# Performance work log

Hardware: AMD Instinct MI355X
Metric: run time of the kernel (lower is better)

The kernel has to match this reference:

```python
import jax, jax.numpy as jnp
import numpy as np

B, S, E, H = 4, 1024, 1024, 16
HD = E // H  # 64


def setup_inputs() -> dict:
    key = jax.random.key(0)
    ks = jax.random.split(key, 9)
    scale = 1.0 / np.sqrt(E)
    x = jax.random.normal(ks[0], (B, S, E), dtype=jnp.float32)
    attention_mask = jnp.ones((B, S, S), dtype=jnp.int32)
    # per-head projection weights, batched over heads: [H, E, HD]
    Wq = jax.random.normal(ks[1], (H, E, HD), dtype=jnp.float32) * scale
    Wk = jax.random.normal(ks[2], (H, E, HD), dtype=jnp.float32) * scale
    Wv = jax.random.normal(ks[3], (H, E, HD), dtype=jnp.float32) * scale
    bq = jax.random.normal(ks[4], (H, HD), dtype=jnp.float32) * scale
    bk = jax.random.normal(ks[5], (H, HD), dtype=jnp.float32) * scale
    bv = jax.random.normal(ks[6], (H, HD), dtype=jnp.float32) * scale
    # output projection, torch Linear convention: [out_features, in_features]
    Wo = jax.random.normal(ks[7], (E, E), dtype=jnp.float32) * scale
    bo = jax.random.normal(ks[8], (E,), dtype=jnp.float32) * scale
    return {"x": x, "attention_mask": attention_mask, "Wq": Wq, "bq": bq,
            "Wk": Wk, "bk": bk, "Wv": Wv, "bv": bv, "Wo": Wo, "bo": bo}


def reference(x, attention_mask, Wq, bq, Wk, bk, Wv, bv, Wo, bo):
    # batched-over-heads QKV projections: (B,S,E) x (H,E,HD) -> (B,H,S,HD)
    q = jnp.einsum('bse,hed->bhsd', x, Wq) + bq[None, :, None, :]
    k = jnp.einsum('bse,hed->bhsd', x, Wk) + bk[None, :, None, :]
    v = jnp.einsum('bse,hed->bhsd', x, Wv) + bv[None, :, None, :]
    scores = jnp.einsum('bhsd,bhtd->bhst', q, k) / jnp.sqrt(jnp.float32(HD))
    mask = attention_mask[:, None, :, :]  # (B,1,S,S) broadcast over heads
    scores = jnp.where(mask == 0, -jnp.inf, scores)
    weights = jax.nn.softmax(scores, axis=-1)
    out = jnp.einsum('bhst,bhtd->bhsd', weights, v)
    # concat heads on last dim: (B,S,H*HD) == (B,S,E)
    out = out.transpose(0, 2, 1, 3).reshape(B, S, E)
    return out @ Wo.T + bo
```

## Files before the change

kernel.cpp:

```cpp
#include <hip/hip_runtime.h>
#include <hip/hip_bf16.h>

#define NB 4
#define SEQ 1024
#define EMB 1024
#define NH 16
#define HD 64

typedef unsigned short u16;
typedef __attribute__((ext_vector_type(8))) __bf16 bf16x8;
typedef __attribute__((ext_vector_type(8))) short short8;
typedef __attribute__((ext_vector_type(4))) float floatx4;

__device__ inline u16 f2b_rn(float f) {
    union { float f; unsigned int i; } x; x.f = f;
    unsigned int r = (x.i + 0x7FFFu + ((x.i >> 16) & 1u)) >> 16;
    return (u16)r;
}
__device__ inline bf16x8 s2b(short8 v) {
    union { short8 s; bf16x8 b; } x; x.s = v; return x.b;
}

__device__ inline void gload_lds16(const void* g, void* l) {
    __builtin_amdgcn_global_load_lds(
        (const __attribute__((address_space(1))) void*)g,
        (__attribute__((address_space(3))) void*)l, 16, 0, 0);
}

__device__ inline bf16x8 ldsfrag(const u16* base, int r, int c) {
    return s2b(*(const short8*)&base[r * 64 + (c ^ ((r & 7) * 8))]);
}

__device__ inline void cvt8(const float* __restrict__ s, u16* __restrict__ d) {
    float4 a = *(const float4*)(s);
    float4 b = *(const float4*)(s + 4);
    union { u16 u[8]; int4 v; } o;
    o.u[0] = f2b_rn(a.x); o.u[1] = f2b_rn(a.y); o.u[2] = f2b_rn(a.z); o.u[3] = f2b_rn(a.w);
    o.u[4] = f2b_rn(b.x); o.u[5] = f2b_rn(b.y); o.u[6] = f2b_rn(b.z); o.u[7] = f2b_rn(b.w);
    *(int4*)(d) = o.v;
}

#define BARX do { __builtin_amdgcn_sched_barrier(0); __builtin_amdgcn_s_barrier(); __builtin_amdgcn_sched_barrier(0); } while(0)
#define VMCNT6 asm volatile("s_waitcnt vmcnt(6)" ::: "memory")
#define VMCNT5 asm volatile("s_waitcnt vmcnt(5)" ::: "memory")
#define VMCNT4 asm volatile("s_waitcnt vmcnt(4)" ::: "memory")
#define VMCNT0 asm volatile("s_waitcnt vmcnt(0)" ::: "memory")

__global__ __launch_bounds__(256) void prep(
    const float* __restrict__ x, const float* __restrict__ Wq,
    const float* __restrict__ Wk, const float* __restrict__ Wv,
    const int* __restrict__ mask,
    u16* __restrict__ xb, u16* __restrict__ Wt,
    unsigned long long* __restrict__ bits)
{
    __shared__ u16 T[64 * 80];
    int bx = blockIdx.x;
    int tid = threadIdx.x;

    if (bx < 512) {
        #pragma unroll
        for (int c = 0; c < 4; ++c) {
            int i = (bx * 4 + c) * 2048 + tid * 8;
            cvt8(x + i, xb + i);
        }
    } else if (bx < 1280) {
        int bx2 = bx - 512;
        int e0 = (bx2 & 15) * 64;
        int ph = bx2 >> 4;
        int p = ph >> 4, h = ph & 15;
        const float* W = (p == 0 ? Wq : (p == 1 ? Wk : Wv)) + h * (EMB * HD);
        #pragma unroll
        for (int c = 0; c < 2; ++c) {
            int flat = c * 2048 + tid * 8;
            int r = flat >> 6;
            int d = flat & 63;
            cvt8(W + (size_t)(e0 + r) * HD + d, &T[r * 80 + d]);
        }
        __syncthreads();
        int d = tid >> 2;
        int ec = tid & 3;
        union { u16 u[16]; int4 v[2]; } tmp;
        #pragma unroll
        for (int i = 0; i < 16; ++i) tmp.u[i] = T[(ec * 16 + i) * 80 + d];
        u16* dst = Wt + ((size_t)(p * NH + h) * HD + d) * EMB + e0 + ec * 16;
        *(int4*)(dst) = tmp.v[0];
        *(int4*)(dst + 8) = tmp.v[1];
    } else {
        int w = tid >> 6, ln = tid & 63;
        int gw = (bx - 1280) * 16 + w * 4 + (ln >> 4);
        int4 v = ((const int4*)mask)[(size_t)gw * 16 + (ln & 15)];
        unsigned nib = (v.x != 0 ? 1u : 0u) | (v.y != 0 ? 2u : 0u)
                     | (v.z != 0 ? 4u : 0u) | (v.w != 0 ? 8u : 0u);
        unsigned long long part = (unsigned long long)nib << ((ln & 15) * 4);
        part |= __shfl_xor(part, 1);
        part |= __shfl_xor(part, 2);
        part |= __shfl_xor(part, 4);
        part |= __shfl_xor(part, 8);
        if ((ln & 15) == 0) bits[gw] = part;
    }
}

__device__ __forceinline__ void rd_b3(const u16* B, int wn, int ln, int quad, bf16x8 (&bfr)[3][2]) {
    #pragma unroll
    for (int nc = 0; nc < 3; ++nc) {
        bfr[nc][0] = ldsfrag(B, wn * 48 + nc * 16 + ln, quad * 8);
        bfr[nc][1] = ldsfrag(B, wn * 48 + nc * 16 + ln, 32 + quad * 8);
    }
}
__device__ __forceinline__ void rd_a(const u16* A, int wm, int mf0, int ln, int quad, bf16x8 (&a)[2][2]) {
    #pragma unroll
    for (int jj = 0; jj < 2; ++jj) {
        a[jj][0] = ldsfrag(A, wm * 128 + (mf0 + jj) * 16 + ln, quad * 8);
        a[jj][1] = ldsfrag(A, wm * 128 + (mf0 + jj) * 16 + ln, 32 + quad * 8);
    }
}
__device__ __forceinline__ void mm12(floatx4 (&acc)[8][3], const bf16x8 (&a)[2][2],
                                     const bf16x8 (&bfr)[3][2], int mf0) {
    #pragma unroll
    for (int jj = 0; jj < 2; ++jj)
        #pragma unroll
        for (int nc = 0; nc < 3; ++nc) {
            acc[mf0 + jj][nc] = __builtin_amdgcn_mfma_f32_16x16x32_bf16(a[jj][0], bfr[nc][0], acc[mf0 + jj][nc], 0, 0, 0);
            acc[mf0 + jj][nc] = __builtin_amdgcn_mfma_f32_16x16x32_bf16(a[jj][1], bfr[nc][1], acc[mf0 + jj][nc], 0, 0, 0);
        }
}

#define STG(srcb, buf, c, kt) gload_lds16((srcb) + (size_t)(c) * 65536 + (kt) * 64 + soff, (buf) + (c) * 4096 + ldst)

__global__ __launch_bounds__(512, 2) void qkv_gemm(
    const u16* __restrict__ x,
    const u16* __restrict__ Wt2,
    const float* __restrict__ bq, const float* __restrict__ bk, const float* __restrict__ bv,
    u16* __restrict__ Q, u16* __restrict__ K, u16* __restrict__ Vt)
{
    __shared__ u16 L[57344];
    u16* A0s = L;
    u16* A1s = L + 16384;
    u16* B0s = L + 32768;
    u16* B1s = L + 45056;

    int gid = blockIdx.x;
    int xcd = gid & 7;
    int j   = gid >> 3;
    int mt_ = (xcd >> 1) * 4 + (j & 3);
    int nt_ = (xcd & 1) * 8 + (j >> 2);
    int m0 = mt_ * 256;
    int n0 = nt_ * 192;

    int tid = threadIdx.x;
    int w = tid >> 6, lane = tid & 63, quad = lane >> 4, ln = lane & 15;
    int wm = w >> 2, wn = w & 3;

    const u16* Asrc = x   + (size_t)m0 * EMB;
    const u16* Bsrc = Wt2 + (size_t)n0 * EMB;

    int sr = tid >> 3;
    int sc = ((tid & 7) ^ (sr & 7)) * 8;
    size_t soff = (size_t)sr * EMB + sc;
    int ldst = w * 512;

    STG(Asrc, A0s, 0, 0); STG(Asrc, A0s, 1, 0); STG(Asrc, A0s, 2, 0); STG(Asrc, A0s, 3, 0);
    STG(Bsrc, B0s, 0, 0); STG(Bsrc, B0s, 1, 0); STG(Bsrc, B0s, 2, 0);
    STG(Bsrc, B1s, 0, 1); STG(Bsrc, B1s, 1, 1); STG(Bsrc, B1s, 2, 1);
    STG(Asrc, A1s, 0, 1); STG(Asrc, A1s, 2, 1);
    VMCNT5;
    BARX;

    floatx4 acc[8][3] = {};
    bf16x8 bfr[3][2];
    bf16x8 a[2][2];

    for (int i = 0; i < 8; ++i) {
        const int T = 2 * i;
        const bool st = (i < 7);
        rd_b3(B0s, wn, ln, quad, bfr);
        rd_a(A0s, wm, 0, ln, quad, a);
        STG(Asrc, A1s, 1, T + 1); STG(Asrc, A1s, 3, T + 1);
        BARX;
        __builtin_amdgcn_s_setprio(1); mm12(acc, a, bfr, 0); __builtin_amdgcn_s_setprio(0);
        BARX;
        rd_a(A0s, wm, 2, ln, quad, a);
        if (st) { STG(Bsrc, B0s, 0, T + 2); STG(Bsrc, B0s, 1, T + 2); }
        BARX;
        __builtin_amdgcn_s_setprio(1); mm12(acc, a, bfr, 2); __builtin_amdgcn_s_setprio(0);
        BARX;
        rd_a(A0s, wm, 4, ln, quad, a);
        if (st) { STG(Bsrc, B0s, 2, T + 2); STG(Asrc, A0s, 0, T + 2); }
        BARX;
        __builtin_amdgcn_s_setprio(1); mm12(acc, a, bfr, 4); __builtin_amdgcn_s_setprio(0);
        BARX;
        rd_a(A0s, wm, 6, ln, quad, a);
        if (st) { STG(Asrc, A0s, 2, T + 2); }
        BARX;
        __builtin_amdgcn_s_setprio(1); mm12(acc, a, bfr, 6); __builtin_amdgcn_s_setprio(0);
        if (st) { VMCNT5; } else { VMCNT0; }
        BARX;
        rd_b3(B1s, wn, ln, quad, bfr);
        rd_a(A1s, wm, 0, ln, quad, a);
        if (st) { STG(Asrc, A0s, 1, T + 2); STG(Asrc, A0s, 3, T + 2); }
        BARX;
        __builtin_amdgcn_s_setprio(1); mm12(acc, a, bfr, 0); __builtin_amdgcn_s_setprio(0);
        BARX;
        rd_a(A1s, wm, 2, ln, quad, a);
        if (st) { STG(Bsrc, B1s, 0, T + 3); STG(Bsrc, B1s, 1, T + 3); }
        BARX;
        __builtin_amdgcn_s_setprio(1); mm12(acc, a, bfr, 2); __builtin_amdgcn_s_setprio(0);
        BARX;
        rd_a(A1s, wm, 4, ln, quad, a);
        if (st) { STG(Bsrc, B1s, 2, T + 3); STG(Asrc, A1s, 0, T + 3); }
        BARX;
        __builtin_amdgcn_s_setprio(1); mm12(acc, a, bfr, 4); __builtin_amdgcn_s_setprio(0);
        BARX;
        rd_a(A1s, wm, 6, ln, quad, a);
        if (st) { STG(Asrc, A1s, 2, T + 3); }
        BARX;
        __builtin_amdgcn_s_setprio(1); mm12(acc, a, bfr, 6); __builtin_amdgcn_s_setprio(0);
        if (st) { VMCNT5; }
        BARX;
    }

    int nb_w = n0 + wn * 48;
    #pragma unroll
    for (int nc = 0; nc < 3; ++nc) {
        int nbc = nb_w + nc * 16;
        int p = nbc >> 10;
        int h = (nbc >> 6) & 15;
        const float* bias = (p == 0 ? bq : (p == 1 ? bk : bv));
        int d = (nbc & 63) + ln;
        float bv_ = bias[(nbc & 1023) + ln];
        if (p < 2) {
            u16* Out = (p == 0) ? Q : K;
            float qs = (p == 0) ? 0.125f * 1.44269504f : 1.0f;
            #pragma unroll
            for (int mf = 0; mf < 8; ++mf) {
                #pragma unroll
                for (int reg = 0; reg < 4; ++reg) {
                    int m = m0 + wm * 128 + mf * 16 + quad * 4 + reg;
                    int b_ = m >> 10, s = m & 1023;
                    Out[((size_t)(b_ * NH + h) * SEQ + s) * HD + d] = f2b_rn((acc[mf][nc][reg] + bv_) * qs);
                }
            }
        } else {
            #pragma unroll
            for (int mf = 0; mf < 8; ++mf) {
                int m = m0 + wm * 128 + mf * 16 + quad * 4;
                int b_ = m >> 10, s = m & 1023;
                union { u16 u[4]; uint2 v; } pk;
                #pragma unroll
                for (int reg = 0; reg < 4; ++reg)
                    pk.u[reg] = f2b_rn(acc[mf][nc][reg] + bv_);
                *(uint2*)&Vt[((size_t)(b_ * NH + h) * HD + d) * SEQ + s] = pk.v;
            }
        }
    }
}

__device__ __forceinline__ void astage512(const u16* __restrict__ Kb, const u16* __restrict__ Vb,
                                          u16* Kd, u16* Vd, int t0, int tid) {
    int r = tid >> 3;
    int c = ((tid & 7) ^ (r & 7)) * 8;
    int base = (tid >> 6) * 512;
    gload_lds16(Kb + (size_t)(t0 + r) * HD + c, Kd + base);
    gload_lds16(Vb + (size_t)r * SEQ + t0 + c, Vd + base);
}

__device__ __forceinline__ void attn_tile(
    const u16* Ksc, const u16* Vsc, u16* Ps,
    const bf16x8 (&qf)[2][2], floatx4 (&o)[2][5],
    unsigned long long bm0, unsigned long long bm1,
    int w, int ln, int quad)
{
    floatx4 sc[2][4] = {};
    #pragma unroll
    for (int kk = 0; kk < 2; ++kk) {
        bf16x8 kf[4];
        #pragma unroll
        for (int tb = 0; tb < 4; ++tb)
            kf[tb] = ldsfrag(Ksc, tb * 16 + ln, kk * 32 + quad * 8);
        __builtin_amdgcn_s_setprio(1);
        #pragma unroll
        for (int s = 0; s < 2; ++s)
            #pragma unroll
            for (int tb = 0; tb < 4; ++tb)
                sc[s][tb] = __builtin_amdgcn_mfma_f32_16x16x32_bf16(kf[tb], qf[s][kk], sc[s][tb], 0, 0, 0);
        __builtin_amdgcn_s_setprio(0);
    }

    #pragma unroll
    for (int s = 0; s < 2; ++s) {
        unsigned long long bm = s ? bm1 : bm0;
        if (__any(bm != ~0ull)) {
            #pragma unroll
            for (int tb = 0; tb < 4; ++tb)
                #pragma unroll
                for (int reg = 0; reg < 4; ++reg)
                    if (!((bm >> (tb * 16 + quad * 4 + reg)) & 1)) sc[s][tb][reg] = -1e30f;
        }
    }

    #pragma unroll
    for (int s = 0; s < 2; ++s) {
        int mrow = w * 32 + s * 16 + ln;
        int swz = (mrow & 7) * 8;
        #pragma unroll
        for (int tb = 0; tb < 4; ++tb) {
            union { float f; unsigned int i; } e0_, e1_, e2_, e3_;
            e0_.f = __builtin_amdgcn_exp2f(sc[s][tb][0]);
            e1_.f = __builtin_amdgcn_exp2f(sc[s][tb][1]);
            e2_.f = __builtin_amdgcn_exp2f(sc[s][tb][2]);
            e3_.f = __builtin_amdgcn_exp2f(sc[s][tb][3]);
            uint2 pk;
            pk.x = ((e0_.i + 0x8000u) >> 16) | ((e1_.i + 0x8000u) & 0xFFFF0000u);
            pk.y = ((e2_.i + 0x8000u) >> 16) | ((e3_.i + 0x8000u) & 0xFFFF0000u);
            *(uint2*)&Ps[mrow * 64 + ((tb * 16 + quad * 4) ^ swz)] = pk;
        }
    }

    #pragma unroll
    for (int kk = 0; kk < 2; ++kk) {
        bf16x8 vf[5];
        #pragma unroll
        for (int dt = 0; dt < 5; ++dt)
            vf[dt] = ldsfrag(Vsc, dt * 16 + ln, kk * 32 + quad * 8);
        #pragma unroll
        for (int s = 0; s < 2; ++s) {
            bf16x8 pf = ldsfrag(Ps, w * 32 + s * 16 + ln, kk * 32 + quad * 8);
            __builtin_amdgcn_s_setprio(1);
            #pragma unroll
            for (int dt = 0; dt < 5; ++dt)
                o[s][dt] = __builtin_amdgcn_mfma_f32_16x16x32_bf16(pf, vf[dt], o[s][dt], 0, 0, 0);
            __builtin_amdgcn_s_setprio(0);
        }
    }
}

__global__ __launch_bounds__(512) void attn(
    const u16* __restrict__ Q, const u16* __restrict__ K, const u16* __restrict__ Vt,
    const unsigned long long* __restrict__ bits,
    const float* __restrict__ Wo, u16* __restrict__ Wob,
    u16* __restrict__ Aout)
{
    __shared__ u16 L[16512 + 256 * 64];
    u16* Ks0 = L;
    u16* Ks1 = L + 4096;
    u16* Vs0 = L + 8192;
    u16* Vs1 = L + 12352;
    u16* Ps  = L + 16512;

    int bid = blockIdx.x;
    int tid = threadIdx.x;

    if (bid >= 256) {
        int i = (bid - 256) * 4096 + tid * 8;
        cvt8(Wo + i, Wob + i);
        return;
    }

    int bh = bid & 63;
    int q0 = (bid >> 6) * 256;
    int b = bh >> 4, h = bh & 15;
    const u16* Qb = Q  + (size_t)bh * SEQ * HD;
    const u16* Kb = K  + (size_t)bh * SEQ * HD;
    const u16* Vb = Vt + (size_t)bh * HD * SEQ;

    int w = tid >> 6, lane = tid & 63, quad = lane >> 4, ln = lane & 15;

    if (tid < 32) {
        u16* dst = (tid < 16 ? L + 12288 : L + 16448) + (tid & 15) * 4;
        *(uint2*)dst = make_uint2(0x3F803F80u, 0x3F803F80u);
    }

    bf16x8 qf[2][2];
    #pragma unroll
    for (int s = 0; s < 2; ++s) {
        const u16* qp = Qb + (size_t)(q0 + w * 32 + s * 16 + ln) * HD + quad * 8;
        union { int4 i; bf16x8 b; } c0, c1;
        c0.i = *(const int4*)(qp);
        c1.i = *(const int4*)(qp + 32);
        qf[s][0] = c0.b; qf[s][1] = c1.b;
    }

    __syncthreads();

    astage512(Kb, Vb, Ks0, Vs0, 0,  tid);
    astage512(Kb, Vb, Ks1, Vs1, 64, tid);
    size_t bb0 = ((size_t)b * SEQ + q0 + w * 32 + ln) * 16;
    size_t bb1 = bb0 + 256;
    unsigned long long bmn0 = bits[bb0];
    unsigned long long bmn1 = bits[bb1];

    floatx4 o[2][5] = {};

    for (int i = 0; i < 8; ++i) {
        VMCNT4;
        BARX;
        {
            unsigned long long bc0 = bmn0, bc1 = bmn1;
            bmn0 = bits[bb0 + (2 * i + 1)];
            bmn1 = bits[bb1 + (2 * i + 1)];
            attn_tile(Ks0, Vs0, Ps, qf, o, bc0, bc1, w, ln, quad);
        }
        BARX;
        if (i < 7) astage512(Kb, Vb, Ks0, Vs0, i * 128 + 128, tid);
        if (i < 7) { VMCNT4; } else { VMCNT0; }
        BARX;
        {
            unsigned long long bc0 = bmn0, bc1 = bmn1;
            if (i < 7) { bmn0 = bits[bb0 + (2 * i + 2)]; bmn1 = bits[bb1 + (2 * i + 2)]; }
            attn_tile(Ks1, Vs1, Ps, qf, o, bc0, bc1, w, ln, quad);
        }
        BARX;
        if (i < 7) astage512(Kb, Vb, Ks1, Vs1, i * 128 + 192, tid);
    }

    #pragma unroll
    for (int s = 0; s < 2; ++s) {
        #pragma unroll
        for (int reg = 0; reg < 4; ++reg) {
            float l = __shfl(o[s][4][reg], lane & 48, 64);
            float inv = 1.0f / l;
            int m = q0 + w * 32 + s * 16 + quad * 4 + reg;
            #pragma unroll
            for (int dt = 0; dt < 4; ++dt)
                Aout[((size_t)b * SEQ + m) * EMB + h * HD + dt * 16 + ln] = f2b_rn(o[s][dt][reg] * inv);
        }
    }
}

#define OSTG_A(buf, kt) gload_lds16(Asrc + (size_t)(kt) * 64 + soff, (buf) + ldst)
#define OSTG_B(buf, c, kt) gload_lds16(Bsrc + (size_t)(c) * 65536 + (size_t)(kt) * 64 + soff, (buf) + (c) * 4096 + ldst)

__device__ __forceinline__ void op_tile(const u16* As, const u16* Bs,
                                        floatx4 (&acc)[4][2], int w, int ln, int quad)
{
    #pragma unroll
    for (int kk = 0; kk < 2; ++kk) {
        bf16x8 av[4], bv2[2];
        #pragma unroll
        for (int mf = 0; mf < 4; ++mf)
            av[mf] = ldsfrag(As, mf * 16 + ln, kk * 32 + quad * 8);
        #pragma unroll
        for (int nc = 0; nc < 2; ++nc)
            bv2[nc] = ldsfrag(Bs, w * 32 + nc * 16 + ln, kk * 32 + quad * 8);
        __builtin_amdgcn_s_setprio(1);
        #pragma unroll
        for (int mf = 0; mf < 4; ++mf)
            #pragma unroll
            for (int nc = 0; nc < 2; ++nc)
                acc[mf][nc] = __builtin_amdgcn_mfma_f32_16x16x32_bf16(av[mf], bv2[nc], acc[mf][nc], 0, 0, 0);
        __builtin_amdgcn_s_setprio(0);
    }
}

__global__ __launch_bounds__(512, 2) void out_proj(
    const u16* __restrict__ A,
    const u16* __restrict__ Wo,
    const float* __restrict__ bo,
    float* __restrict__ Out)
{
    __shared__ u16 L[40960];
    u16* A0s = L;
    u16* A1s = L + 4096;
    u16* B0s = L + 8192;
    u16* B1s = L + 24576;

    int gid = blockIdx.x;
    int xcd = gid & 7;
    int j   = gid >> 3;
    int m0 = (xcd * 8 + (j & 7)) * 64;
    int n0 = (j >> 3) * 256;

    int tid = threadIdx.x;
    int w = tid >> 6, lane = tid & 63, quad = lane >> 4, ln = lane & 15;

    const u16* Asrc = A  + (size_t)m0 * EMB;
    const u16* Bsrc = Wo + (size_t)n0 * EMB;
    int sr = tid >> 3;
    int sc = ((tid & 7) ^ (sr & 7)) * 8;
    size_t soff = (size_t)sr * EMB + sc;
    int ldst = w * 512;

    OSTG_A(A0s, 0); OSTG_B(B0s, 0, 0); OSTG_B(B0s, 1, 0); OSTG_B(B0s, 2, 0); OSTG_B(B0s, 3, 0);
    OSTG_A(A1s, 1); OSTG_B(B1s, 0, 1); OSTG_B(B1s, 1, 1); OSTG_B(B1s, 2, 1); OSTG_B(B1s, 3, 1);

    floatx4 acc[4][2] = {};

    for (int i = 0; i < 8; ++i) {
        VMCNT5;
        BARX;
        op_tile(A0s, B0s, acc, w, ln, quad);
        BARX;
        if (i < 7) {
            int kt = 2 * i + 2;
            OSTG_A(A0s, kt); OSTG_B(B0s, 0, kt); OSTG_B(B0s, 1, kt); OSTG_B(B0s, 2, kt); OSTG_B(B0s, 3, kt);
        }
        if (i < 7) { VMCNT5; } else { VMCNT0; }
        BARX;
        op_tile(A1s, B1s, acc, w, ln, quad);
        BARX;
        if (i < 7) {
            int kt = 2 * i + 3;
            OSTG_A(A1s, kt); OSTG_B(B1s, 0, kt); OSTG_B(B1s, 1, kt); OSTG_B(B1s, 2, kt); OSTG_B(B1s, 3, kt);
        }
    }

    #pragma unroll
    for (int nc = 0; nc < 2; ++nc) {
        int n = n0 + w * 32 + nc * 16 + ln;
        float bb = bo[n];
        #pragma unroll
        for (int mf = 0; mf < 4; ++mf) {
            #pragma unroll
            for (int reg = 0; reg < 4; ++reg) {
                int m = m0 + mf * 16 + quad * 4 + reg;
                Out[(size_t)m * EMB + n] = acc[mf][nc][reg] + bb;
            }
        }
    }
}

extern "C" void kernel_launch(void* const* d_in, const int* in_sizes, int n_in,
                              void* d_out, int out_size, void* d_ws, size_t ws_size,
                              hipStream_t stream) {
    const float* x  = (const float*)d_in[0];
    const int*   mk = (const int*)d_in[1];
    const float* Wq = (const float*)d_in[2];
    const float* bq = (const float*)d_in[3];
    const float* Wk = (const float*)d_in[4];
    const float* bk = (const float*)d_in[5];
    const float* Wv = (const float*)d_in[6];
    const float* bv = (const float*)d_in[7];
    const float* Wo = (const float*)d_in[8];
    const float* bo = (const float*)d_in[9];
    float* out = (float*)d_out;

    const size_t MB = 1u << 20;
    char* ws = (char*)d_ws;
    u16* xb  = (u16*)ws;
    u16* Wt  = (u16*)(ws + 8 * MB);
    u16* Wob = (u16*)(ws + 14 * MB);
    unsigned long long* bits = (unsigned long long*)(ws + 16 * MB);
    u16* Qw  = (u16*)(ws + 16 * MB + 512 * 1024);
    u16* Kw  = (u16*)(ws + 24 * MB + 512 * 1024);
    u16* Vtw = (u16*)(ws + 32 * MB + 512 * 1024);
    u16* Ao  = xb;

    prep<<<5376, 256, 0, stream>>>(x, Wq, Wk, Wv, mk, xb, Wt, bits);
    qkv_gemm<<<256, 512, 0, stream>>>(xb, Wt, bq, bk, bv, Qw, Kw, Vtw);
    attn<<<512, 512, 0, stream>>>(Qw, Kw, Vtw, bits, Wo, Wob, Ao);
    out_proj<<<256, 512, 0, stream>>>(Ao, Wob, bo, out);
}
```

Baseline: 177.8 us.

## Stage two key/value tiles per barrier phase in attention pipeline

```diff
diff --git a/kernel.cpp b/kernel.cpp
--- a/kernel.cpp
+++ b/kernel.cpp
@@ -41,7 +41,7 @@
 }
 
 #define BARX do { __builtin_amdgcn_sched_barrier(0); __builtin_amdgcn_s_barrier(); __builtin_amdgcn_sched_barrier(0); } while(0)
-#define VMCNT6 asm volatile("s_waitcnt vmcnt(6)" ::: "memory")
+#define VMCNT8 asm volatile("s_waitcnt vmcnt(8)" ::: "memory")
 #define VMCNT5 asm volatile("s_waitcnt vmcnt(5)" ::: "memory")
 #define VMCNT4 asm volatile("s_waitcnt vmcnt(4)" ::: "memory")
 #define VMCNT0 asm volatile("s_waitcnt vmcnt(0)" ::: "memory")
@@ -255,13 +255,16 @@
     }
 }
 
-__device__ __forceinline__ void astage512(const u16* __restrict__ Kb, const u16* __restrict__ Vb,
-                                          u16* Kd, u16* Vd, int t0, int tid) {
+__device__ __forceinline__ void stage_pair(const u16* __restrict__ Kb, const u16* __restrict__ Vb,
+                                           u16* Ka, u16* Kb2, u16* Va, u16* Vb2,
+                                           int t0, int tid) {
     int r = tid >> 3;
     int c = ((tid & 7) ^ (r & 7)) * 8;
     int base = (tid >> 6) * 512;
-    gload_lds16(Kb + (size_t)(t0 + r) * HD + c, Kd + base);
-    gload_lds16(Vb + (size_t)r * SEQ + t0 + c, Vd + base);
+    gload_lds16(Kb + (size_t)(t0 + r) * HD + c,       Ka  + base);
+    gload_lds16(Kb + (size_t)(t0 + 64 + r) * HD + c,  Kb2 + base);
+    gload_lds16(Vb + (size_t)r * SEQ + t0 + c,        Va  + base);
+    gload_lds16(Vb + (size_t)r * SEQ + t0 + 64 + c,   Vb2 + base);
 }
 
 __device__ __forceinline__ void attn_tile(
@@ -340,12 +343,17 @@
     const float* __restrict__ Wo, u16* __restrict__ Wob,
     u16* __restrict__ Aout)
 {
-    __shared__ u16 L[16512 + 256 * 64];
-    u16* Ks0 = L;
-    u16* Ks1 = L + 4096;
-    u16* Vs0 = L + 8192;
-    u16* Vs1 = L + 12352;
-    u16* Ps  = L + 16512;
+    __shared__ u16 L[65792];
+    u16* Ks0a = L;
+    u16* Ks0b = L + 4096;
+    u16* Ks1a = L + 8192;
+    u16* Ks1b = L + 12288;
+    u16* Vs0a = L + 16384;
+    u16* Vs0b = L + 20544;
+    u16* Vs1a = L + 24704;
+    u16* Vs1b = L + 28864;
+    u16* Ps_a = L + 33024;
+    u16* Ps_b = L + 49408;
 
     int bid = blockIdx.x;
     int tid = threadIdx.x;
@@ -365,8 +373,9 @@
 
     int w = tid >> 6, lane = tid & 63, quad = lane >> 4, ln = lane & 15;
 
-    if (tid < 32) {
-        u16* dst = (tid < 16 ? L + 12288 : L + 16448) + (tid & 15) * 4;
+    if (tid < 64) {
+        int row = tid >> 4;
+        u16* dst = L + 20480 + row * 4160 + (tid & 15) * 4;
         *(uint2*)dst = make_uint2(0x3F803F80u, 0x3F803F80u);
     }
 
@@ -382,35 +391,36 @@
 
     __syncthreads();
 
-    astage512(Kb, Vb, Ks0, Vs0, 0,  tid);
-    astage512(Kb, Vb, Ks1, Vs1, 64, tid);
+    stage_pair(Kb, Vb, Ks0a, Ks0b, Vs0a, Vs0b, 0,   tid);
+    stage_pair(Kb, Vb, Ks1a, Ks1b, Vs1a, Vs1b, 128, tid);
     size_t bb0 = ((size_t)b * SEQ + q0 + w * 32 + ln) * 16;
     size_t bb1 = bb0 + 256;
-    unsigned long long bmn0 = bits[bb0];
-    unsigned long long bmn1 = bits[bb1];
+    unsigned long long nA0 = bits[bb0 + 0], nA1 = bits[bb1 + 0];
+    unsigned long long nB0 = bits[bb0 + 1], nB1 = bits[bb1 + 1];
 
     floatx4 o[2][5] = {};
 
-    for (int i = 0; i < 8; ++i) {
-        VMCNT4;
+    for (int p = 0; p < 8; ++p) {
+        u16 *Ka, *Kc, *Va, *Vc;
+        if ((p & 1) == 0) { Ka = Ks0a; Kc = Ks0b; Va = Vs0a; Vc = Vs0b; }
+        else              { Ka = Ks1a; Kc = Ks1b; Va = Vs1a; Vc = Vs1b; }
+
+        if (p == 0)      { VMCNT0; }
+        else if (p == 7) { VMCNT4; }
+        else             { VMCNT8; }
         BARX;
         {
-            unsigned long long bc0 = bmn0, bc1 = bmn1;
-            bmn0 = bits[bb0 + (2 * i + 1)];
-            bmn1 = bits[bb1 + (2 * i + 1)];
-            attn_tile(Ks0, Vs0, Ps, qf, o, bc0, bc1, w, ln, quad);
-        }
-        BARX;
-        if (i < 7) astage512(Kb, Vb, Ks0, Vs0, i * 128 + 128, tid);
-        if (i < 7) { VMCNT4; } else { VMCNT0; }
-        BARX;
-        {
-            unsigned long long bc0 = bmn0, bc1 = bmn1;
-            if (i < 7) { bmn0 = bits[bb0 + (2 * i + 2)]; bmn1 = bits[bb1 + (2 * i + 2)]; }
-            attn_tile(Ks1, Vs1, Ps, qf, o, bc0, bc1, w, ln, quad);
-        }
-        BARX;
-        if (i < 7) astage512(Kb, Vb, Ks1, Vs1, i * 128 + 192, tid);
+            unsigned long long cA0 = nA0, cA1 = nA1, cB0 = nB0, cB1 = nB1;
+            if (p < 7) {
+                nA0 = bits[bb0 + 2 * (p + 1)];     nA1 = bits[bb1 + 2 * (p + 1)];
+                nB0 = bits[bb0 + 2 * (p + 1) + 1]; nB1 = bits[bb1 + 2 * (p + 1) + 1];
+            }
+            attn_tile(Ka, Va, Ps_a, qf, o, cA0, cA1, w, ln, quad);
+            attn_tile(Kc, Vc, Ps_b, qf, o, cB0, cB1, w, ln, quad);
+        }
+        BARX;
+        if (p < 6)
+            stage_pair(Kb, Vb, Ka, Kc, Va, Vc, (p + 2) * 128, tid);
     }
 
     #pragma unroll
```

Result: no change. 180.0 us (+1.2%).
